# Optimization experiments

Measured on AMD Instinct MI355X. Metric: run time of the kernel, lower is better.

Reference implementation:

```python
import jax, jax.numpy as jnp
import numpy as np
from itertools import product

GRID_N = 256
N_RAYS, N_SAMPLES = 2048, 128


def setup_inputs() -> dict:
    key = jax.random.key(0)
    k1, k2 = jax.random.split(key)
    sdf_grid = jax.random.normal(k1, (GRID_N, GRID_N, GRID_N), dtype=jnp.float32)
    # monotone voxel-center coordinates over [-1, 1] (sdf_util.get_grid_pts analog)
    x_grid = jnp.linspace(-1.0, 1.0, GRID_N, dtype=jnp.float32)
    y_grid = jnp.linspace(-1.0, 1.0, GRID_N, dtype=jnp.float32)
    z_grid = jnp.linspace(-1.0, 1.0, GRID_N, dtype=jnp.float32)
    # single object pose (sdf_map_pose); identity as in SDFModel.__init__
    pose = jnp.eye(4, dtype=jnp.float32)
    # query sample points in [-0.95, 0.95]^3
    pts = jax.random.uniform(k2, (N_RAYS, N_SAMPLES, 3), dtype=jnp.float32,
                             minval=-0.95, maxval=0.95)
    return {"sdf_grid": sdf_grid, "x_grid": x_grid, "y_grid": y_grid,
            "z_grid": z_grid, "pose": pose, "pts": pts}


def _interp_axis(p, x):
    """Per-dim bucketize + left/right distances (torch.bucketize right=False
    == searchsorted side='left'). p: [N] sorted, x: [K]. Returns idx_l, idx_r,
    dist_l, dist_r, overall, all shape [K]."""
    n = p.shape[0]
    idx_r = jnp.searchsorted(p, x, side="left")
    idx_r = jnp.where(idx_r >= n, n - 1, idx_r)
    idx_l = jnp.clip(idx_r - 1, 0, n - 1)
    dist_l = jnp.maximum(x - p[idx_l], 0.0)
    dist_r = jnp.maximum(p[idx_r] - x, 0.0)
    both_zero = (dist_l == 0.0) & (dist_r == 0.0)
    dist_l = jnp.where(both_zero, 1.0, dist_l)
    dist_r = jnp.where(both_zero, 1.0, dist_r)
    return idx_l, idx_r, dist_l, dist_r, dist_l + dist_r


def reference(sdf_grid, x_grid, y_grid, z_grid, pose, pts):
    # SDFModel.transform with a single pose: x_obj = T_inv @ [x; 1]
    x = pts.reshape(-1, 3)                               # [K, 3]
    T_inv = jnp.linalg.inv(pose)
    x_obj = x @ T_inv[:3, :3].T + T_inv[:3, 3]           # [K, 3]

    grids = (x_grid, y_grid, z_grid)
    axis_data = [_interp_axis(p, x_obj[:, d]) for d, p in enumerate(grids)]
    idxs = [(a[0], a[1]) for a in axis_data]
    dists = [(a[2], a[3]) for a in axis_data]
    overalls = jnp.stack([a[4] for a in axis_data])      # [3, K]

    numerator = jnp.zeros(x.shape[0], dtype=sdf_grid.dtype)
    for indexer in product([0, 1], repeat=3):            # 8 corners
        ix, iy, iz = (idx[onoff] for onoff, idx in zip(indexer, idxs))
        w = (dists[0][1 - indexer[0]] * dists[1][1 - indexer[1]]
             * dists[2][1 - indexer[2]])                  # opposite-side weights
        numerator = numerator + sdf_grid[ix, iy, iz] * w
    denominator = jnp.prod(overalls, axis=0)             # [K]
    return numerator / denominator                       # [K] squeezed SDF
```

## Files before the change

kernel.cpp:

```cpp
#include <hip/hip_runtime.h>

#define GRID_N 256

typedef float float2u __attribute__((ext_vector_type(2), aligned(4)));

__global__ __launch_bounds__(256) void sdf_interp_kernel(
    const float* __restrict__ sdf,
    const float* __restrict__ xg,
    const float* __restrict__ yg,
    const float* __restrict__ zg,
    const float* __restrict__ pose,
    const float* __restrict__ pts,
    float* __restrict__ out,
    int K) {
    __shared__ float sx[GRID_N];
    __shared__ float sy[GRID_N];
    __shared__ float sz[GRID_N];
    __shared__ float ti[12];

    if (threadIdx.x == 0) {
        float a[4][8];
        for (int r = 0; r < 4; ++r)
            for (int c = 0; c < 4; ++c) {
                a[r][c]     = pose[r * 4 + c];
                a[r][c + 4] = (r == c) ? 1.0f : 0.0f;
            }
        for (int c = 0; c < 4; ++c) {
            int piv = c;
            float best = fabsf(a[c][c]);
            for (int r = c + 1; r < 4; ++r) {
                float v = fabsf(a[r][c]);
                if (v > best) { best = v; piv = r; }
            }
            if (piv != c)
                for (int j = 0; j < 8; ++j) {
                    float t = a[c][j]; a[c][j] = a[piv][j]; a[piv][j] = t;
                }
            float inv = 1.0f / a[c][c];
            for (int j = 0; j < 8; ++j) a[c][j] *= inv;
            for (int r = 0; r < 4; ++r) {
                if (r == c) continue;
                float f = a[r][c];
                for (int j = 0; j < 8; ++j) a[r][j] -= f * a[c][j];
            }
        }
        for (int r = 0; r < 3; ++r)
            for (int c = 0; c < 4; ++c)
                ti[r * 4 + c] = a[r][c + 4];
    }
    sx[threadIdx.x] = xg[threadIdx.x];
    sy[threadIdx.x] = yg[threadIdx.x];
    sz[threadIdx.x] = zg[threadIdx.x];
    __syncthreads();

    const int i0 = blockIdx.x * (blockDim.x * 2) + threadIdx.x;
    const int i1 = i0 + 256;

#define FIND(P, V, L, R)                                                  \
    int L, R;                                                             \
    {                                                                     \
        const float p0 = P[0];                                            \
        const float invh = 1.0f / (P[1] - p0);                            \
        int r = (int)ceilf(((V) - p0) * invh);                            \
        r = (r < 0) ? 0 : ((r > GRID_N - 1) ? GRID_N - 1 : r);            \
        while (r > 0 && P[r - 1] >= (V)) --r;                             \
        while (r < GRID_N - 1 && P[r] < (V)) ++r;                         \
        R = r;                                                            \
        L = (r > 0) ? r - 1 : 0;                                          \
    }

#define WEIGHTS(P, V, IL, IR, DL, DR)                                     \
    float DL = fmaxf((V) - P[IL], 0.0f);                                  \
    float DR = fmaxf(P[IR] - (V), 0.0f);                                  \
    if (DL == 0.0f && DR == 0.0f) { DL = 1.0f; DR = 1.0f; }

    float xA, yA, zA;
    int ixlA, ixrA, iylA, iyrA, izlA, izrA;
    float2u a00, a01, a10, a11;
    if (i0 < K) {
        const float px = pts[3 * i0 + 0];
        const float py = pts[3 * i0 + 1];
        const float pz = pts[3 * i0 + 2];
        xA = ti[0] * px + ti[1] * py + ti[2]  * pz + ti[3];
        yA = ti[4] * px + ti[5] * py + ti[6]  * pz + ti[7];
        zA = ti[8] * px + ti[9] * py + ti[10] * pz + ti[11];
        FIND(sx, xA, l0, r0) ixlA = l0; ixrA = r0;
        FIND(sy, yA, l1, r1) iylA = l1; iyrA = r1;
        FIND(sz, zA, l2, r2) izlA = l2; izrA = r2;
        const int bx0 = ixlA * (GRID_N * GRID_N);
        const int bx1 = ixrA * (GRID_N * GRID_N);
        const int by0 = iylA * GRID_N;
        const int by1 = iyrA * GRID_N;
        a00 = __builtin_nontemporal_load((const float2u*)(sdf + bx0 + by0 + izlA));
        a01 = __builtin_nontemporal_load((const float2u*)(sdf + bx0 + by1 + izlA));
        a10 = __builtin_nontemporal_load((const float2u*)(sdf + bx1 + by0 + izlA));
        a11 = __builtin_nontemporal_load((const float2u*)(sdf + bx1 + by1 + izlA));
    }

    float xB, yB, zB;
    int ixlB, ixrB, iylB, iyrB, izlB, izrB;
    float2u b00, b01, b10, b11;
    if (i1 < K) {
        const float px = pts[3 * i1 + 0];
        const float py = pts[3 * i1 + 1];
        const float pz = pts[3 * i1 + 2];
        xB = ti[0] * px + ti[1] * py + ti[2]  * pz + ti[3];
        yB = ti[4] * px + ti[5] * py + ti[6]  * pz + ti[7];
        zB = ti[8] * px + ti[9] * py + ti[10] * pz + ti[11];
        FIND(sx, xB, l0, r0) ixlB = l0; ixrB = r0;
        FIND(sy, yB, l1, r1) iylB = l1; iyrB = r1;
        FIND(sz, zB, l2, r2) izlB = l2; izrB = r2;
        const int bx0 = ixlB * (GRID_N * GRID_N);
        const int bx1 = ixrB * (GRID_N * GRID_N);
        const int by0 = iylB * GRID_N;
        const int by1 = iyrB * GRID_N;
        b00 = __builtin_nontemporal_load((const float2u*)(sdf + bx0 + by0 + izlB));
        b01 = __builtin_nontemporal_load((const float2u*)(sdf + bx0 + by1 + izlB));
        b10 = __builtin_nontemporal_load((const float2u*)(sdf + bx1 + by0 + izlB));
        b11 = __builtin_nontemporal_load((const float2u*)(sdf + bx1 + by1 + izlB));
    }

    if (i0 < K) {
        WEIGHTS(sx, xA, ixlA, ixrA, dlx, drx)
        WEIGHTS(sy, yA, iylA, iyrA, dly, dry)
        WEIGHTS(sz, zA, izlA, izrA, dlz, drz)
        const bool zs = (izrA == izlA);
        const float v000 = a00.x, v001 = zs ? a00.x : a00.y;
        const float v010 = a01.x, v011 = zs ? a01.x : a01.y;
        const float v100 = a10.x, v101 = zs ? a10.x : a10.y;
        const float v110 = a11.x, v111 = zs ? a11.x : a11.y;
        const float numer =
            drx * (dry * (v000 * drz + v001 * dlz) +
                   dly * (v010 * drz + v011 * dlz)) +
            dlx * (dry * (v100 * drz + v101 * dlz) +
                   dly * (v110 * drz + v111 * dlz));
        const float denom = (dlx + drx) * (dly + dry) * (dlz + drz);
        out[i0] = numer / denom;
    }

    if (i1 < K) {
        WEIGHTS(sx, xB, ixlB, ixrB, dlx, drx)
        WEIGHTS(sy, yB, iylB, iyrB, dly, dry)
        WEIGHTS(sz, zB, izlB, izrB, dlz, drz)
        const bool zs = (izrB == izlB);
        const float v000 = b00.x, v001 = zs ? b00.x : b00.y;
        const float v010 = b01.x, v011 = zs ? b01.x : b01.y;
        const float v100 = b10.x, v101 = zs ? b10.x : b10.y;
        const float v110 = b11.x, v111 = zs ? b11.x : b11.y;
        const float numer =
            drx * (dry * (v000 * drz + v001 * dlz) +
                   dly * (v010 * drz + v011 * dlz)) +
            dlx * (dry * (v100 * drz + v101 * dlz) +
                   dly * (v110 * drz + v111 * dlz));
        const float denom = (dlx + drx) * (dly + dry) * (dlz + drz);
        out[i1] = numer / denom;
    }
#undef FIND
#undef WEIGHTS
}

extern "C" void kernel_launch(void* const* d_in, const int* in_sizes, int n_in,
                              void* d_out, int out_size, void* d_ws, size_t ws_size,
                              hipStream_t stream) {
    const float* sdf  = (const float*)d_in[0];
    const float* xg   = (const float*)d_in[1];
    const float* yg   = (const float*)d_in[2];
    const float* zg   = (const float*)d_in[3];
    const float* pose = (const float*)d_in[4];
    const float* pts  = (const float*)d_in[5];
    float* out = (float*)d_out;

    const int K = in_sizes[5] / 3;

    const int block = 256;
    const int grid = (K + block * 2 - 1) / (block * 2);
    sdf_interp_kernel<<<grid, block, 0, stream>>>(sdf, xg, yg, zg, pose, pts,
                                                  out, K);
}
```

Before: 25.79 us.

## Counting-sort query points by (x,y) cell before trilinear gather

Adds a histogram, prefix-scan, and scatter pass that bucket query points by their x/y grid cell, so the gather kernel reads SDF corners from a spatially coherent order and writes results back through an index permutation. The intent is to improve cache locality of the random 64MB grid gathers. It costs four extra launches, a memset, global atomics, a single-block serial scan over 65536 bins, and extra workspace traffic. A fallback unsorted kernel is kept for when the workspace is too small.

```diff
diff --git a/kernel.cpp b/kernel.cpp
--- a/kernel.cpp
+++ b/kernel.cpp
@@ -1,23 +1,12 @@
 #include <hip/hip_runtime.h>
 
 #define GRID_N 256
+#define NBINS  65536
 
 typedef float float2u __attribute__((ext_vector_type(2), aligned(4)));
 
-__global__ __launch_bounds__(256) void sdf_interp_kernel(
-    const float* __restrict__ sdf,
-    const float* __restrict__ xg,
-    const float* __restrict__ yg,
-    const float* __restrict__ zg,
-    const float* __restrict__ pose,
-    const float* __restrict__ pts,
-    float* __restrict__ out,
-    int K) {
-    __shared__ float sx[GRID_N];
-    __shared__ float sy[GRID_N];
-    __shared__ float sz[GRID_N];
-    __shared__ float ti[12];
-
+__device__ __forceinline__ void invert_pose_block(const float* __restrict__ pose,
+                                                  float* ti) {
     if (threadIdx.x == 0) {
         float a[4][8];
         for (int r = 0; r < 4; ++r)
@@ -48,6 +37,88 @@
             for (int c = 0; c < 4; ++c)
                 ti[r * 4 + c] = a[r][c + 4];
     }
+}
+
+__device__ __forceinline__ int bin_key(float x, float y,
+                                       float x0, float invhx,
+                                       float y0, float invhy) {
+    int bx = (int)((x - x0) * invhx);
+    bx = (bx < 0) ? 0 : ((bx > 255) ? 255 : bx);
+    int by = (int)((y - y0) * invhy);
+    by = (by < 0) ? 0 : ((by > 255) ? 255 : by);
+    return (bx << 8) | by;
+}
+
+__global__ __launch_bounds__(256) void hist_kernel(
+    const float* __restrict__ pose, const float* __restrict__ pts,
+    const float* __restrict__ xg, const float* __restrict__ yg,
+    int* __restrict__ hist, int K) {
+    __shared__ float ti[12];
+    invert_pose_block(pose, ti);
+    __syncthreads();
+    const int i = blockIdx.x * blockDim.x + threadIdx.x;
+    if (i >= K) return;
+    const float px = pts[3 * i], py = pts[3 * i + 1], pz = pts[3 * i + 2];
+    const float x = ti[0] * px + ti[1] * py + ti[2] * pz + ti[3];
+    const float y = ti[4] * px + ti[5] * py + ti[6] * pz + ti[7];
+    const float x0 = xg[0], invhx = 1.0f / (xg[1] - x0);
+    const float y0 = yg[0], invhy = 1.0f / (yg[1] - y0);
+    atomicAdd(&hist[bin_key(x, y, x0, invhx, y0, invhy)], 1);
+}
+
+__global__ __launch_bounds__(1024) void prefix_kernel(int* __restrict__ hist) {
+    __shared__ int part[1024];
+    const int t = threadIdx.x;
+    const int base = t * 64;
+    int local[64];
+    int s = 0;
+    for (int j = 0; j < 64; ++j) { local[j] = hist[base + j]; s += local[j]; }
+    part[t] = s;
+    __syncthreads();
+    for (int off = 1; off < 1024; off <<= 1) {
+        int v = (t >= off) ? part[t - off] : 0;
+        __syncthreads();
+        part[t] += v;
+        __syncthreads();
+    }
+    int ex = part[t] - s;
+    for (int j = 0; j < 64; ++j) { int c = local[j]; hist[base + j] = ex; ex += c; }
+}
+
+__global__ __launch_bounds__(256) void scatter_kernel(
+    const float* __restrict__ pose, const float* __restrict__ pts,
+    const float* __restrict__ xg, const float* __restrict__ yg,
+    int* __restrict__ hist, float* __restrict__ spts,
+    int* __restrict__ sidx, int K) {
+    __shared__ float ti[12];
+    invert_pose_block(pose, ti);
+    __syncthreads();
+    const int i = blockIdx.x * blockDim.x + threadIdx.x;
+    if (i >= K) return;
+    const float px = pts[3 * i], py = pts[3 * i + 1], pz = pts[3 * i + 2];
+    const float x = ti[0] * px + ti[1] * py + ti[2] * pz + ti[3];
+    const float y = ti[4] * px + ti[5] * py + ti[6] * pz + ti[7];
+    const float x0 = xg[0], invhx = 1.0f / (xg[1] - x0);
+    const float y0 = yg[0], invhy = 1.0f / (yg[1] - y0);
+    const int key = bin_key(x, y, x0, invhx, y0, invhy);
+    const int slot = atomicAdd(&hist[key], 1);
+    spts[3 * slot + 0] = px;
+    spts[3 * slot + 1] = py;
+    spts[3 * slot + 2] = pz;
+    sidx[slot] = i;
+}
+
+__global__ __launch_bounds__(256) void gather_kernel(
+    const float* __restrict__ sdf,
+    const float* __restrict__ xg, const float* __restrict__ yg,
+    const float* __restrict__ zg, const float* __restrict__ pose,
+    const float* __restrict__ spts, const int* __restrict__ sidx,
+    float* __restrict__ out, int K) {
+    __shared__ float sx[GRID_N];
+    __shared__ float sy[GRID_N];
+    __shared__ float sz[GRID_N];
+    __shared__ float ti[12];
+    invert_pose_block(pose, ti);
     sx[threadIdx.x] = xg[threadIdx.x];
     sy[threadIdx.x] = yg[threadIdx.x];
     sz[threadIdx.x] = zg[threadIdx.x];
@@ -78,9 +149,7 @@
     int ixlA, ixrA, iylA, iyrA, izlA, izrA;
     float2u a00, a01, a10, a11;
     if (i0 < K) {
-        const float px = pts[3 * i0 + 0];
-        const float py = pts[3 * i0 + 1];
-        const float pz = pts[3 * i0 + 2];
+        const float px = spts[3 * i0], py = spts[3 * i0 + 1], pz = spts[3 * i0 + 2];
         xA = ti[0] * px + ti[1] * py + ti[2]  * pz + ti[3];
         yA = ti[4] * px + ti[5] * py + ti[6]  * pz + ti[7];
         zA = ti[8] * px + ti[9] * py + ti[10] * pz + ti[11];
@@ -101,9 +170,7 @@
     int ixlB, ixrB, iylB, iyrB, izlB, izrB;
     float2u b00, b01, b10, b11;
     if (i1 < K) {
-        const float px = pts[3 * i1 + 0];
-        const float py = pts[3 * i1 + 1];
-        const float pz = pts[3 * i1 + 2];
+        const float px = spts[3 * i1], py = spts[3 * i1 + 1], pz = spts[3 * i1 + 2];
         xB = ti[0] * px + ti[1] * py + ti[2]  * pz + ti[3];
         yB = ti[4] * px + ti[5] * py + ti[6]  * pz + ti[7];
         zB = ti[8] * px + ti[9] * py + ti[10] * pz + ti[11];
@@ -135,7 +202,7 @@
             dlx * (dry * (v100 * drz + v101 * dlz) +
                    dly * (v110 * drz + v111 * dlz));
         const float denom = (dlx + drx) * (dly + dry) * (dlz + drz);
-        out[i0] = numer / denom;
+        out[sidx[i0]] = numer / denom;
     }
 
     if (i1 < K) {
@@ -153,10 +220,77 @@
             dlx * (dry * (v100 * drz + v101 * dlz) +
                    dly * (v110 * drz + v111 * dlz));
         const float denom = (dlx + drx) * (dly + dry) * (dlz + drz);
-        out[i1] = numer / denom;
+        out[sidx[i1]] = numer / denom;
     }
 #undef FIND
 #undef WEIGHTS
+}
+
+__global__ __launch_bounds__(256) void sdf_interp_unsorted(
+    const float* __restrict__ sdf,
+    const float* __restrict__ xg, const float* __restrict__ yg,
+    const float* __restrict__ zg, const float* __restrict__ pose,
+    const float* __restrict__ pts, float* __restrict__ out, int K) {
+    __shared__ float sx[GRID_N];
+    __shared__ float sy[GRID_N];
+    __shared__ float sz[GRID_N];
+    __shared__ float ti[12];
+    invert_pose_block(pose, ti);
+    sx[threadIdx.x] = xg[threadIdx.x];
+    sy[threadIdx.x] = yg[threadIdx.x];
+    sz[threadIdx.x] = zg[threadIdx.x];
+    __syncthreads();
+    const int i = blockIdx.x * blockDim.x + threadIdx.x;
+    if (i >= K) return;
+    const float px = pts[3 * i], py = pts[3 * i + 1], pz = pts[3 * i + 2];
+    const float x = ti[0] * px + ti[1] * py + ti[2]  * pz + ti[3];
+    const float y = ti[4] * px + ti[5] * py + ti[6]  * pz + ti[7];
+    const float z = ti[8] * px + ti[9] * py + ti[10] * pz + ti[11];
+#define FIND(P, V, L, R)                                                  \
+    int L, R;                                                             \
+    {                                                                     \
+        const float p0 = P[0];                                            \
+        const float invh = 1.0f / (P[1] - p0);                            \
+        int r = (int)ceilf(((V) - p0) * invh);                            \
+        r = (r < 0) ? 0 : ((r > GRID_N - 1) ? GRID_N - 1 : r);            \
+        while (r > 0 && P[r - 1] >= (V)) --r;                             \
+        while (r < GRID_N - 1 && P[r] < (V)) ++r;                         \
+        R = r;                                                            \
+        L = (r > 0) ? r - 1 : 0;                                          \
+    }
+    FIND(sx, x, ixl, ixr)
+    FIND(sy, y, iyl, iyr)
+    FIND(sz, z, izl, izr)
+#undef FIND
+    const int bx0 = ixl * (GRID_N * GRID_N);
+    const int bx1 = ixr * (GRID_N * GRID_N);
+    const int by0 = iyl * GRID_N;
+    const int by1 = iyr * GRID_N;
+    const float2u z00 = *(const float2u*)(sdf + bx0 + by0 + izl);
+    const float2u z01 = *(const float2u*)(sdf + bx0 + by1 + izl);
+    const float2u z10 = *(const float2u*)(sdf + bx1 + by0 + izl);
+    const float2u z11 = *(const float2u*)(sdf + bx1 + by1 + izl);
+    float dlx = fmaxf(x - sx[ixl], 0.0f);
+    float drx = fmaxf(sx[ixr] - x, 0.0f);
+    if (dlx == 0.0f && drx == 0.0f) { dlx = 1.0f; drx = 1.0f; }
+    float dly = fmaxf(y - sy[iyl], 0.0f);
+    float dry = fmaxf(sy[iyr] - y, 0.0f);
+    if (dly == 0.0f && dry == 0.0f) { dly = 1.0f; dry = 1.0f; }
+    float dlz = fmaxf(z - sz[izl], 0.0f);
+    float drz = fmaxf(sz[izr] - z, 0.0f);
+    if (dlz == 0.0f && drz == 0.0f) { dlz = 1.0f; drz = 1.0f; }
+    const bool zs = (izr == izl);
+    const float v000 = z00.x, v001 = zs ? z00.x : z00.y;
+    const float v010 = z01.x, v011 = zs ? z01.x : z01.y;
+    const float v100 = z10.x, v101 = zs ? z10.x : z10.y;
+    const float v110 = z11.x, v111 = zs ? z11.x : z11.y;
+    const float numer =
+        drx * (dry * (v000 * drz + v001 * dlz) +
+               dly * (v010 * drz + v011 * dlz)) +
+        dlx * (dry * (v100 * drz + v101 * dlz) +
+               dly * (v110 * drz + v111 * dlz));
+    const float denom = (dlx + drx) * (dly + dry) * (dlz + drz);
+    out[i] = numer / denom;
 }
 
 extern "C" void kernel_launch(void* const* d_in, const int* in_sizes, int n_in,
@@ -171,9 +305,29 @@
     float* out = (float*)d_out;
 
     const int K = in_sizes[5] / 3;
+    const size_t need = (size_t)K * 12 + (size_t)K * 4 + (size_t)NBINS * 4;
+
+    if (ws_size < need) {
+        const int block = 256;
+        const int grid = (K + block - 1) / block;
+        sdf_interp_unsorted<<<grid, block, 0, stream>>>(sdf, xg, yg, zg, pose,
+                                                        pts, out, K);
+        return;
+    }
+
+    float* spts = (float*)d_ws;
+    int*   sidx = (int*)((char*)d_ws + (size_t)K * 12);
+    int*   hist = (int*)((char*)d_ws + (size_t)K * 16);
+
+    hipMemsetAsync(hist, 0, (size_t)NBINS * 4, stream);
 
     const int block = 256;
-    const int grid = (K + block * 2 - 1) / (block * 2);
-    sdf_interp_kernel<<<grid, block, 0, stream>>>(sdf, xg, yg, zg, pose, pts,
-                                                  out, K);
-}
+    const int grid1 = (K + block - 1) / block;
+    hist_kernel<<<grid1, block, 0, stream>>>(pose, pts, xg, yg, hist, K);
+    prefix_kernel<<<1, 1024, 0, stream>>>(hist);
+    scatter_kernel<<<grid1, block, 0, stream>>>(pose, pts, xg, yg, hist,
+                                                spts, sidx, K);
+    const int grid2 = (K + block * 2 - 1) / (block * 2);
+    gather_kernel<<<grid2, block, 0, stream>>>(sdf, xg, yg, zg, pose,
+                                               spts, sidx, out, K);
+}
```

New measurement: 79.88 us. 210% more time.
